# Optimization experiments

Hardware: AMD Instinct MI355X
Metric: run time of the kernel (lower is better)

Reference implementation:

```python
import jax, jax.numpy as jnp
import numpy as np
from jax.scipy.special import logsumexp

EPS = 0.1
MAX_ITER = 100
STAB = 1e-6
N_CLASS = 100
BATCH = 4096


def setup_inputs() -> dict:
    key = jax.random.key(0)
    k1, k2 = jax.random.split(key)
    pred = jax.random.normal(k1, (BATCH, N_CLASS), dtype=jnp.float32)
    target = jax.random.randint(k2, (BATCH,), 0, N_CLASS, dtype=jnp.int64)
    return {"pred": pred, "target": target}


def _cost_matrix_euclidean(n_class):
    c = jnp.arange(n_class, dtype=jnp.float32)
    C = (c[None, :] - c[:, None]) ** 2  # [n, n]
    cmax = C.max()
    return jnp.where(cmax > 0, C / cmax, C)


def _sinkhorn_cost(pred, target):
    B, n = pred.shape
    # normalized marginals
    mu = jax.nn.softmax(pred, axis=1) + STAB
    mu = mu / mu.sum(axis=1, keepdims=True)
    nu = jax.nn.one_hot(target, n, dtype=jnp.float32) + STAB
    nu = nu / nu.sum(axis=1, keepdims=True)

    C = _cost_matrix_euclidean(n)               # [n, n]
    K = jnp.exp(-C / EPS)
    log_K = jnp.log(jnp.maximum(K, STAB))       # stabilized kernel

    log_mu = jnp.log(mu + STAB)
    log_nu = jnp.log(nu + STAB)

    def step(carry, _):
        u, v = carry
        # u_new[b,i] = log_mu[b,i] - logsumexp_j(log_K[i,j] + v[b,j])
        u_new = log_mu - logsumexp(log_K[None, :, :] + v[:, None, :], axis=2)
        # v_new[b,j] = log_nu[b,j] - logsumexp_i(log_K[j,i] + u_new[b,i])
        v_new = log_nu - logsumexp(log_K.T[None, :, :] + u_new[:, :, None], axis=1)
        return (u_new, v_new), None

    u0 = jnp.zeros((B, n), dtype=pred.dtype)
    v0 = jnp.zeros((B, n), dtype=pred.dtype)
    (u, v), _ = jax.lax.scan(step, (u0, v0), None, length=MAX_ITER)

    # transport plan with marginal renormalization
    log_P = u[:, :, None] + log_K[None, :, :] + v[:, None, :]
    P = jnp.exp(log_P) + STAB
    P = P / P.sum(axis=2, keepdims=True) * mu[:, :, None]
    P = P / P.sum(axis=1, keepdims=True) * nu[:, None, :]
    cost = jnp.sum(P * C[None, :, :], axis=(1, 2))  # [B]

    # NaN fallback: cost of argmax-to-argmax transport
    alt_cost = C[jnp.argmax(mu, axis=1), jnp.argmax(nu, axis=1)]
    cost = jnp.where(jnp.isnan(cost).any(), alt_cost, cost)
    return cost


def reference(pred, target):
    return _sinkhorn_cost(pred, target).mean()  # reduction='mean'
```

## Files before the change

### kernel.cpp

```cpp
#include <hip/hip_runtime.h>
#include <math.h>

#define NCLS   100
#define ITERS  100
#define RPB    16
#define XS     136
#define XBUF   (RPB * XS)

typedef short  bf16x8 __attribute__((ext_vector_type(8)));
typedef float  f32x4  __attribute__((ext_vector_type(4)));

#if __has_builtin(__builtin_amdgcn_rcpf)
__device__ __forceinline__ float fast_rcp(float x) { return __builtin_amdgcn_rcpf(x); }
#else
__device__ __forceinline__ float fast_rcp(float x) { return 1.0f / x; }
#endif

#if __has_builtin(__builtin_amdgcn_exp2f)
__device__ __forceinline__ float fast_exp2(float x) { return __builtin_amdgcn_exp2f(x); }
#else
__device__ __forceinline__ float fast_exp2(float x) { return exp2f(x); }
#endif

__device__ __forceinline__ unsigned bf16_rne(float f) {
    unsigned u = __float_as_uint(f);
    return (u + 0x7FFFu + ((u >> 16) & 1u)) >> 16;
}
__device__ __forceinline__ float wave_sum(float v) {
#pragma unroll
    for (int m = 32; m > 0; m >>= 1) v += __shfl_xor(v, m, 64);
    return v;
}
__device__ __forceinline__ bool any_ne(f32x4 a, f32x4 b) {
    return (a[0] != b[0]) | (a[1] != b[1]) | (a[2] != b[2]) | (a[3] != b[3]);
}

#define MFMA_B(Af, Bf, Cf) __builtin_amdgcn_mfma_f32_16x16x32_bf16(Af, Bf, Cf, 0, 0, 0)

extern "C" __global__ void sk_zero_out(float* out) { out[0] = 0.0f; }

#define HALF(SRC, DST, MG0, MG1, X0V, X1V)                                   \
    {                                                                        \
        bf16x8 A_[4];                                                        \
        _Pragma("unroll")                                                    \
        for (int s_ = 0; s_ < 4; ++s_)                                       \
            A_[s_] = *(const bf16x8*)((SRC) + lc * XS + s_ * 32 + quad * 8); \
        f32x4 aA_ = {0,0,0,0}, aB_ = {0,0,0,0};                              \
        f32x4 bA_ = {0,0,0,0}, bB_ = {0,0,0,0};                              \
        aA_ = MFMA_B(A_[0], B0[0], aA_);  bA_ = MFMA_B(A_[0], B1[0], bA_);   \
        aB_ = MFMA_B(A_[2], B0[2], aB_);  bB_ = MFMA_B(A_[2], B1[2], bB_);   \
        aA_ = MFMA_B(A_[1], B0[1], aA_);  bA_ = MFMA_B(A_[1], B1[1], bA_);   \
        aB_ = MFMA_B(A_[3], B0[3], aB_);  bB_ = MFMA_B(A_[3], B1[3], bB_);   \
        f32x4 acc0_ = aA_ + aB_;                                             \
        f32x4 acc1_ = bA_ + bB_;                                             \
        _Pragma("unroll")                                                    \
        for (int r_ = 0; r_ < 4; ++r_) {                                     \
            int m_ = quad * 4 + r_;                                          \
            X0V[r_] = MG0[r_] * fast_rcp(acc0_[r_] + bias0);                 \
            X1V[r_] = MG1[r_] * fast_rcp(acc1_[r_] + bias1);                 \
            (DST)[m_ * XS + t0n] = (short)bf16_rne(X0V[r_]);                 \
            (DST)[m_ * XS + t1n] = (short)bf16_rne(X1V[r_]);                 \
        }                                                                    \
        accP0_ = acc0_; accP1_ = acc1_;                                      \
    }

extern "C" __global__ void __launch_bounds__(256)
sk_fused(const float* __restrict__ pred, const int* __restrict__ target,
         float* __restrict__ out, int rows)
{
    __shared__ short xs[2 * XBUF];
    __shared__ __align__(16) float aux[RPB * 104];
    __shared__ int flagS[4];

    const int tid  = threadIdx.x;
    const int lane = tid & 63;
    const int wave = tid >> 6;
    const int quad = lane >> 4;
    const int lc   = lane & 15;
    const int row0 = blockIdx.x * RPB;

    {
        const int r = tid >> 4;
        const int c = tid & 15;
        const float* p = pred + (size_t)(row0 + r) * NCLS;
        const float l2e = 1.44269504089f;
        float v[7];
        float mx = -3.4e38f;
#pragma unroll
        for (int q = 0; q < 7; ++q) {
            int j = c + q * 16;
            v[q] = (j < NCLS) ? p[j] : -3.4e38f;
            mx = fmaxf(mx, v[q]);
        }
#pragma unroll
        for (int m = 8; m >= 1; m >>= 1) mx = fmaxf(mx, __shfl_xor(mx, m, 64));
        float s = 0.f;
#pragma unroll
        for (int q = 0; q < 7; ++q) {
            v[q] = (c + q * 16 < NCLS) ? fast_exp2((v[q] - mx) * l2e) : 0.f;
            s += v[q];
        }
#pragma unroll
        for (int m = 8; m >= 1; m >>= 1) s += __shfl_xor(s, m, 64);
        float invS = 1.f / s;
        float s2 = 0.f;
#pragma unroll
        for (int q = 0; q < 7; ++q) {
            if (c + q * 16 < NCLS) { v[q] = v[q] * invS + 1e-6f; s2 += v[q]; }
        }
#pragma unroll
        for (int m = 8; m >= 1; m >>= 1) s2 += __shfl_xor(s2, m, 64);
        float invM = 1.f / s2;
#pragma unroll
        for (int q = 0; q < 7; ++q) {
            int j = c + q * 16;
            if (j < NCLS) aux[r * 104 + j] = v[q] * invM;
        }
    }

    const int t0n = (2 * wave) * 16 + lc;
    const int t1n = (2 * wave + 1) * 16 + lc;
    const float bias0 = (t0n >= NCLS) ? 1.0f : 0.0f;
    const float bias1 = (t1n >= NCLS) ? 1.0f : 0.0f;

    const float c2 = -14.4269504089f / 9801.0f;
    bf16x8 B0[4], B1[4];
#pragma unroll
    for (int s = 0; s < 4; ++s) {
#pragma unroll
        for (int j = 0; j < 8; ++j) {
            int k  = s * 32 + quad * 8 + j;
            int d0 = k - t0n;
            int d1 = k - t1n;
            B0[s][j] = (short)bf16_rne(fast_exp2(c2 * (float)(d0 * d0)));
            B1[s][j] = (short)bf16_rne(fast_exp2(c2 * (float)(d1 * d1)));
        }
    }

    __syncthreads();

    f32x4 mu0f, mu1f, nu0f, nu1f;
    const float invN = 1.0f / (1.0f + (float)NCLS * 1e-6f);
#pragma unroll
    for (int r = 0; r < 4; ++r) {
        int m = quad * 4 + r;
        mu0f[r] = (t0n < NCLS) ? aux[m * 104 + t0n] : 0.f;
        mu1f[r] = (t1n < NCLS) ? aux[m * 104 + t1n] : 0.f;
        int tg = (int)target[row0 + m];
        nu0f[r] = (t0n < NCLS) ? ((((t0n == tg) ? 1.f : 0.f) + 1e-6f) * invN) : 0.f;
        nu1f[r] = (t1n < NCLS) ? ((((t1n == tg) ? 1.f : 0.f) + 1e-6f) * invN) : 0.f;
    }

#pragma unroll
    for (int r = 0; r < 4; ++r) {
        int m = quad * 4 + r;
        xs[m * XS + t0n] = (short)bf16_rne(nu0f[r]);
        xs[m * XS + t1n] = (short)bf16_rne(nu1f[r]);
    }
    __syncthreads();

    f32x4 pvO0 = {-1.f,-1.f,-1.f,-1.f}, pvO1 = pvO0;
    f32x4 xT0, xT1, accP0_, accP1_;
    for (int pair = 0; pair < ITERS - 1; ++pair) {
        HALF(xs, xs + XBUF, mu0f, mu1f, xT0, xT1);
        __syncthreads();
        HALF(xs + XBUF, xs, nu0f, nu1f, xT0, xT1);
        bool chgO = any_ne(accP0_, pvO0) || any_ne(accP1_, pvO1);
        pvO0 = accP0_; pvO1 = accP1_;
        int anyv = __any((int)chgO);
        if (lane == 0) flagS[wave] = anyv;
        __syncthreads();
        if ((flagS[0] | flagS[1] | flagS[2] | flagS[3]) == 0) break;
    }

    f32x4 aR0, aR1, bR0, bR1;
    HALF(xs, xs + XBUF, mu0f, mu1f, aR0, aR1);
    __syncthreads();
    HALF(xs + XBUF, xs, nu0f, nu1f, bR0, bR1);
    __syncthreads();

    f32x4 t0a = {0.f, 0.f, 0.f, 0.f};
    f32x4 t1a = {0.f, 0.f, 0.f, 0.f};
    {
        bf16x8 A[4];
#pragma unroll
        for (int s = 0; s < 4; ++s)
            A[s] = *(const bf16x8*)(xs + lc * XS + s * 32 + quad * 8);
#pragma unroll
        for (int s = 0; s < 4; ++s) {
            t0a = MFMA_B(A[s], B0[s], t0a);
            t1a = MFMA_B(A[s], B1[s], t1a);
        }
    }

    float* SsumP = aux;
    float* zP    = aux + 64;
    short* sclS  = (short*)(aux + 128);
    short* apS   = xs + XBUF;

#pragma unroll
    for (int r = 0; r < 4; ++r) {
        int m = quad * 4 + r;
        float scl0 = mu0f[r] * fast_rcp(fmaf(aR0[r], t0a[r], (float)NCLS * 1e-6f));
        float scl1 = mu1f[r] * fast_rcp(fmaf(aR1[r], t1a[r], (float)NCLS * 1e-6f));
        apS[m * XS + t0n]  = (short)bf16_rne(aR0[r] * scl0);
        apS[m * XS + t1n]  = (short)bf16_rne(aR1[r] * scl1);
        sclS[m * XS + t0n] = (short)bf16_rne(scl0);
        sclS[m * XS + t1n] = (short)bf16_rne(scl1);
        float ps = scl0 + scl1;
#pragma unroll
        for (int w = 8; w >= 1; w >>= 1) ps += __shfl_xor(ps, w, 64);
        if (lc == 0) SsumP[wave * 16 + m] = ps;
    }
    __syncthreads();

    f32x4 Ssum;
#pragma unroll
    for (int r = 0; r < 4; ++r) {
        int m = quad * 4 + r;
        Ssum[r] = SsumP[m] + SsumP[16 + m] + SsumP[32 + m] + SsumP[48 + m];
    }

    bf16x8 KC0[4], KC1[4], C0[4], C1[4];
    const float cinv = 1.0f / 9801.0f;
#pragma unroll
    for (int s = 0; s < 4; ++s) {
#pragma unroll
        for (int j = 0; j < 8; ++j) {
            int k  = s * 32 + quad * 8 + j;
            int d0 = k - t0n;
            int d1 = k - t1n;
            float c0 = (float)(d0 * d0) * cinv;
            float c1 = (float)(d1 * d1) * cinv;
            KC0[s][j] = (short)bf16_rne(fast_exp2(c2 * (float)(d0 * d0)) * c0);
            KC1[s][j] = (short)bf16_rne(fast_exp2(c2 * (float)(d1 * d1)) * c1);
            C0[s][j]  = (short)bf16_rne(c0);
            C1[s][j]  = (short)bf16_rne(c1);
        }
    }

    f32x4 q0 = {0,0,0,0}, q1 = {0,0,0,0};
    f32x4 m0 = {0,0,0,0}, m1 = {0,0,0,0};
    f32x4 s0 = {0,0,0,0}, s1 = {0,0,0,0};
    {
        bf16x8 Aa[4], As[4];
#pragma unroll
        for (int s = 0; s < 4; ++s) {
            Aa[s] = *(const bf16x8*)(apS  + lc * XS + s * 32 + quad * 8);
            As[s] = *(const bf16x8*)(sclS + lc * XS + s * 32 + quad * 8);
        }
#pragma unroll
        for (int s = 0; s < 4; ++s) {
            q0 = MFMA_B(Aa[s], B0[s],  q0);
            q1 = MFMA_B(Aa[s], B1[s],  q1);
            m0 = MFMA_B(Aa[s], KC0[s], m0);
            m1 = MFMA_B(Aa[s], KC1[s], m1);
            s0 = MFMA_B(As[s], C0[s],  s0);
            s1 = MFMA_B(As[s], C1[s],  s1);
        }
    }

    float z = 0.f;
#pragma unroll
    for (int r = 0; r < 4; ++r) {
        float col0 = fmaf(bR0[r], q0[r], 1e-6f * Ssum[r]);
        float col1 = fmaf(bR1[r], q1[r], 1e-6f * Ssum[r]);
        float in0  = fmaf(bR0[r], m0[r], 1e-6f * s0[r]);
        float in1  = fmaf(bR1[r], m1[r], 1e-6f * s1[r]);
        z += nu0f[r] * fast_rcp(col0) * in0 + nu1f[r] * fast_rcp(col1) * in1;
    }
    z = wave_sum(z);
    if (lane == 0) zP[wave] = z;
    __syncthreads();
    if (tid == 0) {
        float tot = zP[0] + zP[1] + zP[2] + zP[3];
        atomicAdd(out, tot / (float)rows);
    }
}

extern "C" void kernel_launch(void* const* d_in, const int* in_sizes, int n_in,
                              void* d_out, int out_size, void* d_ws, size_t ws_size,
                              hipStream_t stream)
{
    const float* pred   = (const float*)d_in[0];
    const int*   target = (const int*)d_in[1];
    float*       out    = (float*)d_out;
    const int    rows   = in_sizes[0] / NCLS;

    hipLaunchKernelGGL(sk_zero_out, dim3(1), dim3(1), 0, stream, out);
    hipLaunchKernelGGL(sk_fused, dim3(rows / RPB), dim3(256), 0, stream,
                       pred, target, out, rows);
}
```

Measured before the change: 66.99 us.

## Split column tiles across eight waves instead of four per block

Blocks now run 512 threads (eight waves), and each wave owns one 16-column tile instead of two. This halves the per-wave MFMA chain and register footprint inside the serial Sinkhorn iteration loop, aiming to shorten per-iteration latency. The cost is more waves taking part in every block-wide barrier, with flags packed into a byte array that is read as one 64-bit word. The softmax prologue is limited to the first 256 threads, and the reductions and aux offsets are resized for eight waves.

```diff
diff --git a/kernel.cpp b/kernel.cpp
--- a/kernel.cpp
+++ b/kernel.cpp
@@ -39,38 +39,34 @@
 
 extern "C" __global__ void sk_zero_out(float* out) { out[0] = 0.0f; }
 
-#define HALF(SRC, DST, MG0, MG1, X0V, X1V)                                   \
+#define HALF(SRC, DST, MG0, X0V)                                             \
     {                                                                        \
         bf16x8 A_[4];                                                        \
         _Pragma("unroll")                                                    \
         for (int s_ = 0; s_ < 4; ++s_)                                       \
             A_[s_] = *(const bf16x8*)((SRC) + lc * XS + s_ * 32 + quad * 8); \
         f32x4 aA_ = {0,0,0,0}, aB_ = {0,0,0,0};                              \
-        f32x4 bA_ = {0,0,0,0}, bB_ = {0,0,0,0};                              \
-        aA_ = MFMA_B(A_[0], B0[0], aA_);  bA_ = MFMA_B(A_[0], B1[0], bA_);   \
-        aB_ = MFMA_B(A_[2], B0[2], aB_);  bB_ = MFMA_B(A_[2], B1[2], bB_);   \
-        aA_ = MFMA_B(A_[1], B0[1], aA_);  bA_ = MFMA_B(A_[1], B1[1], bA_);   \
-        aB_ = MFMA_B(A_[3], B0[3], aB_);  bB_ = MFMA_B(A_[3], B1[3], bB_);   \
+        aA_ = MFMA_B(A_[0], B0[0], aA_);                                     \
+        aB_ = MFMA_B(A_[2], B0[2], aB_);                                     \
+        aA_ = MFMA_B(A_[1], B0[1], aA_);                                     \
+        aB_ = MFMA_B(A_[3], B0[3], aB_);                                     \
         f32x4 acc0_ = aA_ + aB_;                                             \
-        f32x4 acc1_ = bA_ + bB_;                                             \
         _Pragma("unroll")                                                    \
         for (int r_ = 0; r_ < 4; ++r_) {                                     \
             int m_ = quad * 4 + r_;                                          \
             X0V[r_] = MG0[r_] * fast_rcp(acc0_[r_] + bias0);                 \
-            X1V[r_] = MG1[r_] * fast_rcp(acc1_[r_] + bias1);                 \
             (DST)[m_ * XS + t0n] = (short)bf16_rne(X0V[r_]);                 \
-            (DST)[m_ * XS + t1n] = (short)bf16_rne(X1V[r_]);                 \
         }                                                                    \
-        accP0_ = acc0_; accP1_ = acc1_;                                      \
-    }
-
-extern "C" __global__ void __launch_bounds__(256)
+        accP0_ = acc0_;                                                      \
+    }
+
+extern "C" __global__ void __launch_bounds__(512, 2)
 sk_fused(const float* __restrict__ pred, const int* __restrict__ target,
          float* __restrict__ out, int rows)
 {
     __shared__ short xs[2 * XBUF];
     __shared__ __align__(16) float aux[RPB * 104];
-    __shared__ int flagS[4];
+    __shared__ __align__(8) unsigned char flagC[8];
 
     const int tid  = threadIdx.x;
     const int lane = tid & 63;
@@ -79,7 +75,7 @@
     const int lc   = lane & 15;
     const int row0 = blockIdx.x * RPB;
 
-    {
+    if (tid < 256) {
         const int r = tid >> 4;
         const int c = tid & 15;
         const float* p = pred + (size_t)(row0 + r) * NCLS;
@@ -118,96 +114,84 @@
         }
     }
 
-    const int t0n = (2 * wave) * 16 + lc;
-    const int t1n = (2 * wave + 1) * 16 + lc;
+    const int t0n = wave * 16 + lc;
     const float bias0 = (t0n >= NCLS) ? 1.0f : 0.0f;
-    const float bias1 = (t1n >= NCLS) ? 1.0f : 0.0f;
 
     const float c2 = -14.4269504089f / 9801.0f;
-    bf16x8 B0[4], B1[4];
+    bf16x8 B0[4];
 #pragma unroll
     for (int s = 0; s < 4; ++s) {
 #pragma unroll
         for (int j = 0; j < 8; ++j) {
             int k  = s * 32 + quad * 8 + j;
             int d0 = k - t0n;
-            int d1 = k - t1n;
             B0[s][j] = (short)bf16_rne(fast_exp2(c2 * (float)(d0 * d0)));
-            B1[s][j] = (short)bf16_rne(fast_exp2(c2 * (float)(d1 * d1)));
-        }
-    }
-
-    __syncthreads();
-
-    f32x4 mu0f, mu1f, nu0f, nu1f;
+        }
+    }
+
+    __syncthreads();
+
+    f32x4 mu0f, nu0f;
     const float invN = 1.0f / (1.0f + (float)NCLS * 1e-6f);
 #pragma unroll
     for (int r = 0; r < 4; ++r) {
         int m = quad * 4 + r;
         mu0f[r] = (t0n < NCLS) ? aux[m * 104 + t0n] : 0.f;
-        mu1f[r] = (t1n < NCLS) ? aux[m * 104 + t1n] : 0.f;
         int tg = (int)target[row0 + m];
         nu0f[r] = (t0n < NCLS) ? ((((t0n == tg) ? 1.f : 0.f) + 1e-6f) * invN) : 0.f;
-        nu1f[r] = (t1n < NCLS) ? ((((t1n == tg) ? 1.f : 0.f) + 1e-6f) * invN) : 0.f;
     }
 
 #pragma unroll
     for (int r = 0; r < 4; ++r) {
         int m = quad * 4 + r;
         xs[m * XS + t0n] = (short)bf16_rne(nu0f[r]);
-        xs[m * XS + t1n] = (short)bf16_rne(nu1f[r]);
-    }
-    __syncthreads();
-
-    f32x4 pvO0 = {-1.f,-1.f,-1.f,-1.f}, pvO1 = pvO0;
-    f32x4 xT0, xT1, accP0_, accP1_;
+    }
+    __syncthreads();
+
+    f32x4 pvO0 = {-1.f, -1.f, -1.f, -1.f};
+    f32x4 xT0, accP0_;
     for (int pair = 0; pair < ITERS - 1; ++pair) {
-        HALF(xs, xs + XBUF, mu0f, mu1f, xT0, xT1);
+        HALF(xs, xs + XBUF, mu0f, xT0);
         __syncthreads();
-        HALF(xs + XBUF, xs, nu0f, nu1f, xT0, xT1);
-        bool chgO = any_ne(accP0_, pvO0) || any_ne(accP1_, pvO1);
-        pvO0 = accP0_; pvO1 = accP1_;
+        HALF(xs + XBUF, xs, nu0f, xT0);
+        bool chgO = any_ne(accP0_, pvO0);
+        pvO0 = accP0_;
         int anyv = __any((int)chgO);
-        if (lane == 0) flagS[wave] = anyv;
+        if (lane == 0) flagC[wave] = (unsigned char)anyv;
         __syncthreads();
-        if ((flagS[0] | flagS[1] | flagS[2] | flagS[3]) == 0) break;
-    }
-
-    f32x4 aR0, aR1, bR0, bR1;
-    HALF(xs, xs + XBUF, mu0f, mu1f, aR0, aR1);
-    __syncthreads();
-    HALF(xs + XBUF, xs, nu0f, nu1f, bR0, bR1);
-    __syncthreads();
+        if (*(const unsigned long long*)flagC == 0ULL) break;
+    }
+
+    f32x4 aR0, bR0, accT;
+    HALF(xs, xs + XBUF, mu0f, aR0);
+    __syncthreads();
+    HALF(xs + XBUF, xs, nu0f, bR0);
+    __syncthreads();
+    (void)accT;
 
     f32x4 t0a = {0.f, 0.f, 0.f, 0.f};
-    f32x4 t1a = {0.f, 0.f, 0.f, 0.f};
     {
         bf16x8 A[4];
 #pragma unroll
         for (int s = 0; s < 4; ++s)
             A[s] = *(const bf16x8*)(xs + lc * XS + s * 32 + quad * 8);
 #pragma unroll
-        for (int s = 0; s < 4; ++s) {
+        for (int s = 0; s < 4; ++s)
             t0a = MFMA_B(A[s], B0[s], t0a);
-            t1a = MFMA_B(A[s], B1[s], t1a);
-        }
     }
 
     float* SsumP = aux;
-    float* zP    = aux + 64;
-    short* sclS  = (short*)(aux + 128);
+    float* zP    = aux + 128;
+    short* sclS  = (short*)(aux + 136);
     short* apS   = xs + XBUF;
 
 #pragma unroll
     for (int r = 0; r < 4; ++r) {
         int m = quad * 4 + r;
         float scl0 = mu0f[r] * fast_rcp(fmaf(aR0[r], t0a[r], (float)NCLS * 1e-6f));
-        float scl1 = mu1f[r] * fast_rcp(fmaf(aR1[r], t1a[r], (float)NCLS * 1e-6f));
         apS[m * XS + t0n]  = (short)bf16_rne(aR0[r] * scl0);
-        apS[m * XS + t1n]  = (short)bf16_rne(aR1[r] * scl1);
         sclS[m * XS + t0n] = (short)bf16_rne(scl0);
-        sclS[m * XS + t1n] = (short)bf16_rne(scl1);
-        float ps = scl0 + scl1;
+        float ps = scl0;
 #pragma unroll
         for (int w = 8; w >= 1; w >>= 1) ps += __shfl_xor(ps, w, 64);
         if (lc == 0) SsumP[wave * 16 + m] = ps;
@@ -218,10 +202,13 @@
 #pragma unroll
     for (int r = 0; r < 4; ++r) {
         int m = quad * 4 + r;
-        Ssum[r] = SsumP[m] + SsumP[16 + m] + SsumP[32 + m] + SsumP[48 + m];
-    }
-
-    bf16x8 KC0[4], KC1[4], C0[4], C1[4];
+        float acc = 0.f;
+#pragma unroll
+        for (int w = 0; w < 8; ++w) acc += SsumP[w * 16 + m];
+        Ssum[r] = acc;
+    }
+
+    bf16x8 KC0[4], C0[4];
     const float cinv = 1.0f / 9801.0f;
 #pragma unroll
     for (int s = 0; s < 4; ++s) {
@@ -229,19 +216,13 @@
         for (int j = 0; j < 8; ++j) {
             int k  = s * 32 + quad * 8 + j;
             int d0 = k - t0n;
-            int d1 = k - t1n;
-            float c0 = (float)(d0 * d0) * cinv;
-            float c1 = (float)(d1 * d1) * cinv;
-            KC0[s][j] = (short)bf16_rne(fast_exp2(c2 * (float)(d0 * d0)) * c0);
-            KC1[s][j] = (short)bf16_rne(fast_exp2(c2 * (float)(d1 * d1)) * c1);
-            C0[s][j]  = (short)bf16_rne(c0);
-            C1[s][j]  = (short)bf16_rne(c1);
-        }
-    }
-
-    f32x4 q0 = {0,0,0,0}, q1 = {0,0,0,0};
-    f32x4 m0 = {0,0,0,0}, m1 = {0,0,0,0};
-    f32x4 s0 = {0,0,0,0}, s1 = {0,0,0,0};
+            float cc = (float)(d0 * d0) * cinv;
+            KC0[s][j] = (short)bf16_rne(fast_exp2(c2 * (float)(d0 * d0)) * cc);
+            C0[s][j]  = (short)bf16_rne(cc);
+        }
+    }
+
+    f32x4 qv = {0,0,0,0}, mv = {0,0,0,0}, sv = {0,0,0,0};
     {
         bf16x8 Aa[4], As[4];
 #pragma unroll
@@ -251,29 +232,24 @@
         }
 #pragma unroll
         for (int s = 0; s < 4; ++s) {
-            q0 = MFMA_B(Aa[s], B0[s],  q0);
-            q1 = MFMA_B(Aa[s], B1[s],  q1);
-            m0 = MFMA_B(Aa[s], KC0[s], m0);
-            m1 = MFMA_B(Aa[s], KC1[s], m1);
-            s0 = MFMA_B(As[s], C0[s],  s0);
-            s1 = MFMA_B(As[s], C1[s],  s1);
+            qv = MFMA_B(Aa[s], B0[s],  qv);
+            mv = MFMA_B(Aa[s], KC0[s], mv);
+            sv = MFMA_B(As[s], C0[s],  sv);
         }
     }
 
     float z = 0.f;
 #pragma unroll
     for (int r = 0; r < 4; ++r) {
-        float col0 = fmaf(bR0[r], q0[r], 1e-6f * Ssum[r]);
-        float col1 = fmaf(bR1[r], q1[r], 1e-6f * Ssum[r]);
-        float in0  = fmaf(bR0[r], m0[r], 1e-6f * s0[r]);
-        float in1  = fmaf(bR1[r], m1[r], 1e-6f * s1[r]);
-        z += nu0f[r] * fast_rcp(col0) * in0 + nu1f[r] * fast_rcp(col1) * in1;
+        float col0 = fmaf(bR0[r], qv[r], 1e-6f * Ssum[r]);
+        float in0  = fmaf(bR0[r], mv[r], 1e-6f * sv[r]);
+        z += nu0f[r] * fast_rcp(col0) * in0;
     }
     z = wave_sum(z);
     if (lane == 0) zP[wave] = z;
     __syncthreads();
     if (tid == 0) {
-        float tot = zP[0] + zP[1] + zP[2] + zP[3];
+        float tot = zP[0] + zP[1] + zP[2] + zP[3] + zP[4] + zP[5] + zP[6] + zP[7];
         atomicAdd(out, tot / (float)rows);
     }
 }
@@ -288,6 +264,6 @@
     const int    rows   = in_sizes[0] / NCLS;
 
     hipLaunchKernelGGL(sk_zero_out, dim3(1), dim3(1), 0, stream, out);
-    hipLaunchKernelGGL(sk_fused, dim3(rows / RPB), dim3(256), 0, stream,
+    hipLaunchKernelGGL(sk_fused, dim3(rows / RPB), dim3(512), 0, stream,
                        pred, target, out, rows);
 }
```

Result: no change. 66.19 us (-1.2%).
